# Kernel tuning notes

Hardware: AMD Instinct MI355X
Metric: run time of the kernel (lower is better)

Reference implementation:

```python
import jax, jax.numpy as jnp
import numpy as np
from jax import lax

B, T, HID = 4, 1024, 1024
H, DK, DV = 8, 128, 128
KCONV = 4
EPS = 1e-6
KEY_DIM = H * DK          # 1024
VAL_DIM = H * DV          # 1024
CONV_DIM = 2 * KEY_DIM + VAL_DIM  # 3072


def setup_inputs() -> dict:
    key = jax.random.key(0)
    ks = jax.random.split(key, 11)
    s = 0.02
    return {
        "hidden_states": jax.random.normal(ks[0], (B, T, HID), jnp.float32),
        "qkv_w": jax.random.normal(ks[1], (CONV_DIM, HID), jnp.float32) * s,
        "z_w": jax.random.normal(ks[2], (VAL_DIM, HID), jnp.float32) * s,
        "b_w": jax.random.normal(ks[3], (H, HID), jnp.float32) * s,
        "a_w": jax.random.normal(ks[4], (H, HID), jnp.float32) * s,
        "conv_w": jax.random.normal(ks[5], (CONV_DIM, 1, KCONV), jnp.float32) * 0.2,
        "dt_bias": jnp.ones((H,), jnp.float32),
        "A_log": jnp.log(jax.random.uniform(ks[6], (H,), jnp.float32, 1e-3, 16.0)),
        "norm_w": jnp.ones((DV,), jnp.float32),
        "out_w": jax.random.normal(ks[7], (HID, VAL_DIM), jnp.float32) * s,
    }


def reference(hidden_states, qkv_w, z_w, b_w, a_w, conv_w, dt_bias, A_log, norm_w, out_w):
    b_, t_, _ = hidden_states.shape

    # qkv projection -> [B, T, CONV_DIM]
    mixed = jnp.einsum("bth,ch->btc", hidden_states, qkv_w)

    # causal depthwise conv1d over time (groups == channels, padding K-1, truncated)
    x = mixed.transpose(0, 2, 1)  # [B, C, T]
    x = lax.conv_general_dilated(
        x, conv_w, window_strides=(1,), padding=[(KCONV - 1, 0)],
        feature_group_count=CONV_DIM,
        dimension_numbers=("NCH", "OIH", "NCH"))
    mixed = x.transpose(0, 2, 1)  # [B, T, C]

    z = jnp.einsum("bth,vh->btv", hidden_states, z_w).reshape(b_, t_, H, DV)
    bb = jnp.einsum("bth,nh->btn", hidden_states, b_w)   # [B,T,H]
    aa = jnp.einsum("bth,nh->btn", hidden_states, a_w)   # [B,T,H]

    q, k, v = jnp.split(mixed, 3, axis=-1)
    q = q.reshape(b_, t_, H, DK)
    k = k.reshape(b_, t_, H, DK)
    v = v.reshape(b_, t_, H, DV)

    beta = jax.nn.sigmoid(bb)                                  # [B,T,H]
    g = -jnp.exp(A_log) * jax.nn.softplus(aa + dt_bias)        # [B,T,H]
    alpha = jnp.exp(g)                                         # per-step decay

    # gated delta rule recurrence, time-major scan
    def step(S, inp):
        q_t, k_t, v_t, beta_t, alpha_t = inp  # [B,H,dk],[B,H,dk],[B,H,dv],[B,H],[B,H]
        S = S * alpha_t[..., None, None]                       # decay state
        kv = jnp.einsum("bhk,bhkv->bhv", k_t, S)              # retrieved memory
        S = S + jnp.einsum("bhk,bhv->bhkv", k_t, (v_t - kv) * beta_t[..., None])
        o_t = jnp.einsum("bhk,bhkv->bhv", q_t, S)
        return S, o_t

    qt = q.transpose(1, 0, 2, 3)
    kt = k.transpose(1, 0, 2, 3)
    vt = v.transpose(1, 0, 2, 3)
    bt = beta.transpose(1, 0, 2)
    at = alpha.transpose(1, 0, 2)
    S0 = jnp.zeros((b_, H, DK, DV), hidden_states.dtype)
    _, o = lax.scan(step, S0, (qt, kt, vt, bt, at))            # o: [T,B,H,dv]
    o = o.transpose(1, 0, 2, 3)                                # [B,T,H,dv]

    # gated RMSNorm: rmsnorm(o) * weight * silu(z)
    var = jnp.mean(jnp.square(o), axis=-1, keepdims=True)
    o = o * lax.rsqrt(var + EPS) * norm_w
    o = o * (z * jax.nn.sigmoid(z))

    out = jnp.einsum("btv,hv->bth", o.reshape(b_, t_, VAL_DIM), out_w)
    return out
```

## Files before the change

### kernel.cpp

```cpp
#include <hip/hip_runtime.h>

#define B_ 4
#define T_ 1024
#define HID_ 1024
#define H_ 8
#define CONV_DIM_ 3072
#define MROWS (B_*T_)

typedef __bf16 bf16x8 __attribute__((ext_vector_type(8)));
typedef float f32x4 __attribute__((ext_vector_type(4)));

#define MFMA16(a,b,c) __builtin_amdgcn_mfma_f32_16x16x32_bf16((a),(b),(c),0,0,0)

static __device__ __forceinline__ unsigned short f2bf(float f) {
  unsigned u = __float_as_uint(f);
  unsigned r = u + 0x7fffu + ((u >> 16) & 1u);
  return (unsigned short)(r >> 16);
}
static __device__ __forceinline__ float bfu2f(unsigned short v) {
  return __uint_as_float(((unsigned)v) << 16);
}
static __device__ __forceinline__ float4 recon4(ushort4 h, ushort4 l) {
  float4 r;
  r.x = bfu2f(h.x) + bfu2f(l.x);
  r.y = bfu2f(h.y) + bfu2f(l.y);
  r.z = bfu2f(h.z) + bfu2f(l.z);
  r.w = bfu2f(h.w) + bfu2f(l.w);
  return r;
}

static __device__ __forceinline__ void gld16(void* lds, const void* g) {
  __builtin_amdgcn_global_load_lds(
      (const __attribute__((address_space(1))) unsigned int*)g,
      (__attribute__((address_space(3))) unsigned int*)lds, 16, 0, 0);
}

__global__ __launch_bounds__(256) void f2bf_kernel(
    const float* __restrict__ src, unsigned short* __restrict__ dst, int n) {
  int i = (blockIdx.x * 256 + threadIdx.x) * 4;
  if (i >= n) return;
  float4 v = *(const float4*)(src + i);
  ushort4 o;
  o.x = f2bf(v.x); o.y = f2bf(v.y); o.z = f2bf(v.z); o.w = f2bf(v.w);
  *(ushort4*)(dst + i) = o;
}

__global__ __launch_bounds__(256) void f2bf_split_kernel(
    const float* __restrict__ src, unsigned short* __restrict__ hi,
    unsigned short* __restrict__ lo, int n) {
  int i = (blockIdx.x * 256 + threadIdx.x) * 4;
  if (i >= n) return;
  float4 v = *(const float4*)(src + i);
  ushort4 h, l;
  h.x = f2bf(v.x); h.y = f2bf(v.y); h.z = f2bf(v.z); h.w = f2bf(v.w);
  l.x = f2bf(v.x - bfu2f(h.x));
  l.y = f2bf(v.y - bfu2f(h.y));
  l.z = f2bf(v.z - bfu2f(h.z));
  l.w = f2bf(v.w - bfu2f(h.w));
  *(ushort4*)(hi + i) = h;
  *(ushort4*)(lo + i) = l;
}

template<int OUT_BF16>
__global__ __launch_bounds__(256) void gemm_mfma_kernel(
    const unsigned short* __restrict__ A, const unsigned short* __restrict__ W,
    void* __restrict__ Cv, int M, int N, int K) {
  __shared__ __align__(16) unsigned short lA[128*32];
  __shared__ __align__(16) unsigned short lB[128*32];
  const int tid  = threadIdx.x;
  const int lane = tid & 63;
  const int wv   = tid >> 6;
  const int wm   = (wv >> 1) * 64;
  const int wn   = (wv & 1) * 64;
  const int m16  = lane & 15;
  const int quad = lane >> 4;
  const int bm = blockIdx.y * 128;
  const int bn = blockIdx.x * 128;

  f32x4 acc[4][4];
  #pragma unroll
  for (int i = 0; i < 4; ++i)
    #pragma unroll
    for (int j = 0; j < 4; ++j)
      acc[i][j] = (f32x4){0.f, 0.f, 0.f, 0.f};

  const int r0 = tid >> 2, c0 = tid & 3;
  const int r1 = r0 + 64;
  const int g0 = (c0 ^ (r0 & 3)) * 8;
  const int g1 = (c0 ^ (r1 & 3)) * 8;
  const unsigned short* Ar0 = A + (size_t)(bm + r0) * K + g0;
  const unsigned short* Ar1 = A + (size_t)(bm + r1) * K + g1;
  const unsigned short* Wr0 = W + (size_t)(bn + r0) * K + g0;
  const unsigned short* Wr1 = W + (size_t)(bn + r1) * K + g1;
  unsigned short* sA0 = &lA[(size_t)tid * 8];
  unsigned short* sA1 = &lA[(size_t)(tid + 256) * 8];
  unsigned short* sB0 = &lB[(size_t)tid * 8];
  unsigned short* sB1 = &lB[(size_t)(tid + 256) * 8];

  int offA[4], offB[4];
  #pragma unroll
  for (int i = 0; i < 4; ++i) {
    int ra = wm + i * 16 + m16;
    offA[i] = ra * 32 + (quad ^ (ra & 3)) * 8;
    int rb = wn + i * 16 + m16;
    offB[i] = rb * 32 + (quad ^ (rb & 3)) * 8;
  }

  for (int k0 = 0; k0 < K; k0 += 32) {
    gld16(sA0, Ar0 + k0);
    gld16(sA1, Ar1 + k0);
    gld16(sB0, Wr0 + k0);
    gld16(sB1, Wr1 + k0);
    __syncthreads();
    bf16x8 af[4], bfr[4];
    #pragma unroll
    for (int i = 0; i < 4; ++i) {
      af[i]  = *(const bf16x8*)&lA[offA[i]];
      bfr[i] = *(const bf16x8*)&lB[offB[i]];
    }
    #pragma unroll
    for (int mi = 0; mi < 4; ++mi)
      #pragma unroll
      for (int ni = 0; ni < 4; ++ni)
        acc[mi][ni] = MFMA16(af[mi], bfr[ni], acc[mi][ni]);
    __syncthreads();
  }

  #pragma unroll
  for (int mi = 0; mi < 4; ++mi) {
    #pragma unroll
    for (int r = 0; r < 4; ++r) {
      size_t row = (size_t)(bm + wm + mi * 16 + quad * 4 + r);
      #pragma unroll
      for (int ni = 0; ni < 4; ++ni) {
        int col = bn + wn + ni * 16 + m16;
        float val = acc[mi][ni][r];
        if (OUT_BF16) ((unsigned short*)Cv)[row * N + col] = f2bf(val);
        else          ((float*)Cv)[row * N + col] = val;
      }
    }
  }
}

__global__ __launch_bounds__(256) void gemm_split_conv_kernel(
    const unsigned short* __restrict__ Ahi, const unsigned short* __restrict__ Alo,
    const unsigned short* __restrict__ Whi, const unsigned short* __restrict__ Wlo,
    const float* __restrict__ conv_w,
    unsigned short* __restrict__ qhi, unsigned short* __restrict__ qlo,
    unsigned short* __restrict__ khi, unsigned short* __restrict__ klo,
    float* __restrict__ vb, float* __restrict__ edge) {
  __shared__ __align__(16) unsigned char ldsraw[64*132*4 + 3*128*4];
  unsigned short* lAh = (unsigned short*)ldsraw;
  unsigned short* lAl = lAh + 128*32;
  unsigned short* lBh = lAl + 128*32;
  unsigned short* lBl = lBh + 128*32;
  float* smX2  = (float*)ldsraw;
  float* carry = (float*)(ldsraw + 64*132*4);

  const int tid  = threadIdx.x;
  const int lane = tid & 63;
  const int wv   = tid >> 6;
  const int wm   = (wv >> 1) * 64;
  const int wn   = (wv & 1) * 64;
  const int m16  = lane & 15;
  const int quad = lane >> 4;
  const int bm = blockIdx.y * 128;
  const int bn = blockIdx.x * 128;

  f32x4 acc[4][4];
  #pragma unroll
  for (int i = 0; i < 4; ++i)
    #pragma unroll
    for (int j = 0; j < 4; ++j)
      acc[i][j] = (f32x4){0.f, 0.f, 0.f, 0.f};

  const int r0 = tid >> 2, c0 = tid & 3;
  const int r1 = r0 + 64;
  const int g0 = (c0 ^ (r0 & 3)) * 8;
  const int g1 = (c0 ^ (r1 & 3)) * 8;
  const size_t oA0 = (size_t)(bm + r0) * 1024 + g0;
  const size_t oA1 = (size_t)(bm + r1) * 1024 + g1;
  const size_t oB0 = (size_t)(bn + r0) * 1024 + g0;
  const size_t oB1 = (size_t)(bn + r1) * 1024 + g1;
  const int s0 = tid * 8, s1 = (tid + 256) * 8;

  int offA[4], offB[4];
  #pragma unroll
  for (int i = 0; i < 4; ++i) {
    int ra = wm + i * 16 + m16;
    offA[i] = ra * 32 + (quad ^ (ra & 3)) * 8;
    int rb = wn + i * 16 + m16;
    offB[i] = rb * 32 + (quad ^ (rb & 3)) * 8;
  }

  for (int k0 = 0; k0 < 1024; k0 += 32) {
    gld16(&lAh[s0], Ahi + oA0 + k0);
    gld16(&lAh[s1], Ahi + oA1 + k0);
    gld16(&lAl[s0], Alo + oA0 + k0);
    gld16(&lAl[s1], Alo + oA1 + k0);
    gld16(&lBh[s0], Whi + oB0 + k0);
    gld16(&lBh[s1], Whi + oB1 + k0);
    gld16(&lBl[s0], Wlo + oB0 + k0);
    gld16(&lBl[s1], Wlo + oB1 + k0);
    __syncthreads();
    bf16x8 afh[4], bfh[4];
    #pragma unroll
    for (int i = 0; i < 4; ++i) {
      afh[i] = *(const bf16x8*)&lAh[offA[i]];
      bfh[i] = *(const bf16x8*)&lBh[offB[i]];
    }
    #pragma unroll
    for (int mi = 0; mi < 4; ++mi)
      #pragma unroll
      for (int ni = 0; ni < 4; ++ni)
        acc[mi][ni] = MFMA16(afh[mi], bfh[ni], acc[mi][ni]);
    {
      bf16x8 bfl[4];
      #pragma unroll
      for (int i = 0; i < 4; ++i) bfl[i] = *(const bf16x8*)&lBl[offB[i]];
      #pragma unroll
      for (int mi = 0; mi < 4; ++mi)
        #pragma unroll
        for (int ni = 0; ni < 4; ++ni)
          acc[mi][ni] = MFMA16(afh[mi], bfl[ni], acc[mi][ni]);
    }
    {
      bf16x8 afl[4];
      #pragma unroll
      for (int i = 0; i < 4; ++i) afl[i] = *(const bf16x8*)&lAl[offA[i]];
      #pragma unroll
      for (int mi = 0; mi < 4; ++mi)
        #pragma unroll
        for (int ni = 0; ni < 4; ++ni)
          acc[mi][ni] = MFMA16(afl[mi], bfh[ni], acc[mi][ni]);
    }
    __syncthreads();
  }

  const int bi = blockIdx.y;
  const int c  = tid & 127;
  const int rh = tid >> 7;
  const int cg = bn + c;
  const int part = cg >> 10;
  const int hh = (cg & 1023) >> 7;
  const int b = bm >> 10;
  const int tloc0 = bm & 1023;
  float4 w4 = *(const float4*)(conv_w + cg * 4);
  size_t rowb = ((size_t)(b * H_ + hh)) * T_;
  unsigned short* dh = (part == 0) ? qhi : khi;
  unsigned short* dl = (part == 0) ? qlo : klo;

  #pragma unroll
  for (int half = 0; half < 2; ++half) {
    if (half == 1) __syncthreads();
    if ((wv >> 1) == half) {
      #pragma unroll
      for (int mi = 0; mi < 4; ++mi)
        #pragma unroll
        for (int r = 0; r < 4; ++r) {
          int row = mi * 16 + quad * 4 + r;
          #pragma unroll
          for (int ni = 0; ni < 4; ++ni)
            smX2[row * 132 + wn + ni * 16 + m16] = acc[mi][ni][r];
        }
    }
    __syncthreads();
    if (half == 0) {
      #pragma unroll
      for (int e = 0; e < 2; ++e) {
        int idx = e * 256 + tid;
        int r = idx >> 7, cc = idx & 127;
        if (r < 3) {
          edge[((size_t)bi*6 + 3 + r)*3072 + bn + cc] = smX2[r*132 + cc];
          carry[r*128 + cc] = smX2[(61+r)*132 + cc];
        }
      }
    } else {
      if (bi < 31) {
        #pragma unroll
        for (int e = 0; e < 2; ++e) {
          int idx = e * 256 + tid;
          int r = idx >> 7, cc = idx & 127;
          if (r < 3)
            edge[((size_t)(bi+1)*6 + r)*3072 + bn + cc] = smX2[(61+r)*132 + cc];
        }
      }
    }
    {
      const int tb0 = rh * 32;
      float x0, x1, x2;
      if (tb0 >= 3) {
        x0 = smX2[(tb0-3)*132 + c];
        x1 = smX2[(tb0-2)*132 + c];
        x2 = smX2[(tb0-1)*132 + c];
      } else {
        if (half == 0) { x0 = 0.f; x1 = 0.f; x2 = 0.f; }
        else { x0 = carry[0*128 + c]; x1 = carry[1*128 + c]; x2 = carry[2*128 + c]; }
      }
      for (int tt = 0; tt < 32; ++tt) {
        const int t = tb0 + tt;
        float x3 = smX2[t*132 + c];
        float s = fmaf(w4.x, x0, fmaf(w4.y, x1, fmaf(w4.z, x2, w4.w * x3)));
        x0 = x1; x1 = x2; x2 = x3;
        const int tg = tloc0 + half*64 + t;
        if (part == 2) {
          vb[(rowb + tg) * 128 + c] = s;
        } else {
          int sw = (((c >> 3) ^ (tg & 7)) << 3) + (c & 7);
          unsigned short hv = f2bf(s);
          dh[(rowb + tg) * 128 + sw] = hv;
          dl[(rowb + tg) * 128 + sw] = f2bf(s - bfu2f(hv));
        }
      }
    }
  }
}

__global__ __launch_bounds__(128) void conv_fix_kernel(
    const float* __restrict__ edge, const float* __restrict__ conv_w,
    unsigned short* __restrict__ qhi, unsigned short* __restrict__ qlo,
    unsigned short* __restrict__ khi, unsigned short* __restrict__ klo,
    float* __restrict__ vb) {
  const int bi = blockIdx.x / 24;
  const int cb = blockIdx.x % 24;
  const int bm = bi * 128, n0 = cb * 128;
  const int b = bm >> 10, tloc = bm & 1023;
  const int c = threadIdx.x;
  const int cg = n0 + c;
  float m[6];
  #pragma unroll
  for (int j = 0; j < 6; ++j)
    m[j] = edge[((size_t)bi*6 + j)*3072 + cg];
  if (tloc == 0) { m[0] = 0.f; m[1] = 0.f; m[2] = 0.f; }
  const int part = cg >> 10;
  const int hh = (cg & 1023) >> 7;
  float4 w4 = *(const float4*)(conv_w + cg * 4);
  size_t rowb = ((size_t)(b * H_ + hh)) * T_;
  unsigned short* dh = (part == 0) ? qhi : khi;
  unsigned short* dl = (part == 0) ? qlo : klo;
  #pragma unroll
  for (int jo = 0; jo < 3; ++jo) {
    float s = fmaf(w4.x, m[jo], fmaf(w4.y, m[jo+1],
              fmaf(w4.z, m[jo+2], w4.w * m[jo+3])));
    const int tg = tloc + jo;
    if (part == 2) {
      vb[(rowb + tg) * 128 + c] = s;
    } else {
      int sw = (((c >> 3) ^ (tg & 7)) << 3) + (c & 7);
      unsigned short hv = f2bf(s);
      dh[(rowb + tg) * 128 + sw] = hv;
      dl[(rowb + tg) * 128 + sw] = f2bf(s - bfu2f(hv));
    }
  }
}

__global__ __launch_bounds__(128) void proj_ba_kernel(
    const float* __restrict__ hs, const float* __restrict__ b_w, const float* __restrict__ a_w,
    const float* __restrict__ dt_bias, const float* __restrict__ A_log,
    float* __restrict__ gout, float* __restrict__ beta,
    unsigned short* __restrict__ hs_hi, unsigned short* __restrict__ hs_lo) {
  const int bt = blockIdx.x;
  const int b = bt >> 10;
  const int t = bt & 1023;
  const int tid = threadIdx.x;
  const int grp = tid >> 3;
  const int l8 = tid & 7;
  const int h = grp & 7;
  const bool isA = grp >= 8;
  const float* w = (isA ? a_w : b_w) + (size_t)h * HID_;
  const float* x = hs + (size_t)bt * HID_;
  {
    const int e = tid * 8;
    float4 xv0 = *(const float4*)(x + e);
    float4 xv1 = *(const float4*)(x + e + 4);
    ushort4 h0, l0, h1, l1;
    h0.x = f2bf(xv0.x); h0.y = f2bf(xv0.y); h0.z = f2bf(xv0.z); h0.w = f2bf(xv0.w);
    l0.x = f2bf(xv0.x - bfu2f(h0.x)); l0.y = f2bf(xv0.y - bfu2f(h0.y));
    l0.z = f2bf(xv0.z - bfu2f(h0.z)); l0.w = f2bf(xv0.w - bfu2f(h0.w));
    h1.x = f2bf(xv1.x); h1.y = f2bf(xv1.y); h1.z = f2bf(xv1.z); h1.w = f2bf(xv1.w);
    l1.x = f2bf(xv1.x - bfu2f(h1.x)); l1.y = f2bf(xv1.y - bfu2f(h1.y));
    l1.z = f2bf(xv1.z - bfu2f(h1.z)); l1.w = f2bf(xv1.w - bfu2f(h1.w));
    unsigned short* hho = hs_hi + (size_t)bt * HID_ + e;
    unsigned short* hlo = hs_lo + (size_t)bt * HID_ + e;
    *(ushort4*)hho = h0;       *(ushort4*)hlo = l0;
    *(ushort4*)(hho + 4) = h1; *(ushort4*)(hlo + 4) = l1;
  }
  float s = 0.f;
  for (int e = l8*4; e < HID_; e += 32){
    float4 xv = *(const float4*)(x + e);
    float4 wv = *(const float4*)(w + e);
    s = fmaf(xv.x, wv.x, s);
    s = fmaf(xv.y, wv.y, s);
    s = fmaf(xv.z, wv.z, s);
    s = fmaf(xv.w, wv.w, s);
  }
  s += __shfl_xor(s,1); s += __shfl_xor(s,2); s += __shfl_xor(s,4);
  if (l8 == 0) {
    size_t o = ((size_t)(b*H_ + h))*T_ + t;
    if (!isA) {
      beta[o] = 1.f/(1.f+expf(-s));
    } else {
      float xx = s + dt_bias[h];
      float sp = fmaxf(xx,0.f) + log1pf(expf(-fabsf(xx)));
      gout[o] = -expf(A_log[h]) * sp;
    }
  }
}

__global__ __launch_bounds__(256) void scan_ab_kernel(
    const unsigned short* __restrict__ qhi_g, const unsigned short* __restrict__ qlo_g,
    const unsigned short* __restrict__ khi_g, const unsigned short* __restrict__ klo_g,
    const float* __restrict__ gbuf, const float* __restrict__ bbuf,
    unsigned short* __restrict__ Thi_g, unsigned short* __restrict__ Tlo_g,
    unsigned short* __restrict__ Bhi_g, unsigned short* __restrict__ Blo_g) {
  const int blk = blockIdx.x;
  const int bh = blk >> 4;
  const int ch = blk & 15;
  const int t0 = ch * 64;
  const int tid = threadIdx.x;
  __shared__ float sK[64][132];
  __shared__ float sAA[64][68];
  __shared__ float lL[64];
  __shared__ float bL[64];
  unsigned short* Tho = Thi_g + (size_t)blk*4096;
  unsigned short* Tlo = Tlo_g + (size_t)blk*4096;
  unsigned short* Bho = Bhi_g + (size_t)blk*4096;
  unsigned short* Blo = Blo_g + (size_t)blk*4096;

  #pragma unroll
  for (int i = 0; i < 8; ++i) {
    int f4 = tid + 256*i;
    int row = f4 >> 5, c4 = (f4 & 31) * 4;
    int gr = t0 + row;
    size_t base = ((size_t)bh*1024 + gr)*128;
    int sw = (((c4>>3) ^ (gr&7)) << 3) + (c4 & 7);
    ushort4 h = *(const ushort4*)&khi_g[base + sw];
    ushort4 l = *(const ushort4*)&klo_g[base + sw];
    *(float4*)&sK[row][c4] = recon4(h, l);
  }
  if (tid < 64) {
    float x = gbuf[(size_t)bh*T_ + t0 + tid];
    #pragma unroll
    for (int o = 1; o < 64; o <<= 1) {
      float y = __shfl_up(x, o);
      if (tid >= o) x += y;
    }
    lL[tid] = x;
    bL[tid] = bbuf[(size_t)bh*T_ + t0 + tid];
  }
  __syncthreads();

  const int it = tid >> 4, jt = tid & 15;
  {
    float acc[4][4] = {};
    if (jt <= it) {
      for (int kk = 0; kk < 128; kk += 4) {
        float4 ka[4], kc[4];
        #pragma unroll
        for (int r = 0; r < 4; ++r) {
          ka[r] = *(const float4*)&sK[it*4+r][kk];
          kc[r] = *(const float4*)&sK[jt*4+r][kk];
        }
        #pragma unroll
        for (int a = 0; a < 4; ++a)
          #pragma unroll
          for (int b = 0; b < 4; ++b) {
            acc[a][b] = fmaf(ka[a].x, kc[b].x, acc[a][b]);
            acc[a][b] = fmaf(ka[a].y, kc[b].y, acc[a][b]);
            acc[a][b] = fmaf(ka[a].z, kc[b].z, acc[a][b]);
            acc[a][b] = fmaf(ka[a].w, kc[b].w, acc[a][b]);
          }
      }
    }
    #pragma unroll
    for (int a = 0; a < 4; ++a) {
      int i = it*4 + a;
      float bi = bL[i], li = lL[i];
      #pragma unroll
      for (int b = 0; b < 4; ++b) {
        int j = jt*4 + b;
        sAA[i][j] = (j < i) ? bi * __expf(li - lL[j]) * acc[a][b] : 0.f;
      }
    }
  }
  {
    float acc[4][4] = {};
    if (jt <= it) {
      size_t qbase[4]; int qrx[4];
      #pragma unroll
      for (int r = 0; r < 4; ++r) {
        int gr = t0 + it*4 + r;
        qbase[r] = ((size_t)bh*1024 + gr)*128;
        qrx[r] = gr & 7;
      }
      for (int kk = 0; kk < 128; kk += 4) {
        float4 qa[4], kc[4];
        #pragma unroll
        for (int r = 0; r < 4; ++r) {
          int sw = (((kk>>3) ^ qrx[r]) << 3) + (kk & 7);
          ushort4 h = *(const ushort4*)&qhi_g[qbase[r] + sw];
          ushort4 l = *(const ushort4*)&qlo_g[qbase[r] + sw];
          qa[r] = recon4(h, l);
          kc[r] = *(const float4*)&sK[jt*4+r][kk];
        }
        #pragma unroll
        for (int a = 0; a < 4; ++a)
          #pragma unroll
          for (int b = 0; b < 4; ++b) {
            acc[a][b] = fmaf(qa[a].x, kc[b].x, acc[a][b]);
            acc[a][b] = fmaf(qa[a].y, kc[b].y, acc[a][b]);
            acc[a][b] = fmaf(qa[a].z, kc[b].z, acc[a][b]);
            acc[a][b] = fmaf(qa[a].w, kc[b].w, acc[a][b]);
          }
      }
    }
    #pragma unroll
    for (int a = 0; a < 4; ++a) {
      int i = it*4 + a;
      float li = lL[i];
      #pragma unroll
      for (int b = 0; b < 4; ++b) {
        int j = jt*4 + b;
        float x = (j <= i) ? __expf(li - lL[j]) * acc[a][b] : 0.f;
        unsigned short hv = f2bf(x);
        int sidx = i*64 + (((j>>3) ^ (i&7)) << 3) + (j&7);
        Bho[sidx] = hv;
        Blo[sidx] = f2bf(x - bfu2f(hv));
      }
    }
  }
  __syncthreads();

  {
    const int w = tid >> 6;
    const int ln = tid & 63;
    const int colc = w*16 + (ln & 15);
    const int rr = ln >> 4;
    float rh[16];
    #pragma unroll
    for (int m=0;m<16;++m) rh[m] = (rr + 4*m == colc) ? 1.f : 0.f;
    for (int j = 0; j < 63; ++j) {
      int src = ((j & 3) << 4) | (ln & 15);
      float wj = __shfl(rh[j >> 2], src);
      #pragma unroll
      for (int m=0;m<16;++m)
        rh[m] = fmaf(-sAA[rr + 4*m][j], wj, rh[m]);
    }
    #pragma unroll
    for (int m=0;m<16;++m) {
      int i2 = rr + 4*m;
      float x = rh[m];
      unsigned short hv = f2bf(x);
      int sidx = i2*64 + (((colc>>3) ^ (i2&7)) << 3) + (colc&7);
      Tho[sidx] = hv;
      Tlo[sidx] = f2bf(x - bfu2f(hv));
    }
  }
}

__global__ __launch_bounds__(512) void scan_seq_kernel(
    const unsigned short* __restrict__ khi_g, const unsigned short* __restrict__ klo_g,
    const unsigned short* __restrict__ qhi_g, const unsigned short* __restrict__ qlo_g,
    const float* __restrict__ vb,
    const float* __restrict__ gbuf, const float* __restrict__ bbuf,
    const unsigned short* __restrict__ Thi_g, const unsigned short* __restrict__ Tlo_g,
    const unsigned short* __restrict__ Bhi_g, const unsigned short* __restrict__ Blo_g,
    float* __restrict__ ob) {
  const int bh = blockIdx.x & 31;
  const int sl = blockIdx.x >> 5;
  const int tid = threadIdx.x;
  const int wv = tid >> 6;
  const int lane = tid & 63;
  const int v16 = lane & 15;
  const int quad = lane >> 4;
  const int tb = (wv & 3) * 16;
  const bool isQ = (wv >= 4);
  const int vx = v16 & 7;

  __shared__ __align__(16) unsigned short KhiL[2][64*128];
  __shared__ __align__(16) unsigned short KloL[2][64*128];
  __shared__ __align__(16) unsigned short WTh[16*64],  WTl[16*64];
  __shared__ __align__(16) unsigned short W2Th[16*64], W2Tl[16*64];
  __shared__ __align__(16) unsigned short W3Th[16*64], W3Tl[16*64];
  __shared__ __align__(16) unsigned short S0h[16*128], S0l[16*128];

  const unsigned short* kh  = khi_g + (size_t)bh*131072;
  const unsigned short* klp = klo_g + (size_t)bh*131072;
  const unsigned short* qh  = qhi_g + (size_t)bh*131072;
  const unsigned short* qlp = qlo_g + (size_t)bh*131072;
  const float* vg = vb + (size_t)bh*T_*128 + sl*16;
  const float* gg = gbuf + (size_t)bh*T_;
  const float* beg = bbuf + (size_t)bh*T_;
  float* og = ob + (size_t)bh*T_*128 + sl*16;

  f32x4 sreg = (f32x4){0.f, 0.f, 0.f, 0.f};
  const int kk0 = wv*16 + v16;
  const int k8 = kk0 >> 3, k7 = kk0 & 7;
  const int kq4 = (quad & 1) * 4;
  const int kr8 = (wv*16 + quad*4) >> 3;

  gld16(&KhiL[0][tid*8],        kh + tid*8);
  gld16(&KhiL[0][4096 + tid*8], kh + 4096 + tid*8);
  gld16(&KloL[0][tid*8],        klp + tid*8);
  gld16(&KloL[0][4096 + tid*8], klp + 4096 + tid*8);

  for (int ch = 0; ch < 16; ++ch) {
    const int t0 = ch * 64;
    const int cur = ch & 1;
    __syncthreads();

    if (ch < 15) {
      const size_t co = (size_t)(t0 + 64) * 128;
      gld16(&KhiL[cur^1][tid*8],        kh + co + tid*8);
      gld16(&KhiL[cur^1][4096 + tid*8], kh + co + 4096 + tid*8);
      gld16(&KloL[cur^1][tid*8],        klp + co + tid*8);
      gld16(&KloL[cur^1][4096 + tid*8], klp + co + 4096 + tid*8);
    }

    float gv = gg[t0 + lane];
    #pragma unroll
    for (int o = 1; o < 64; o <<= 1) {
      float y = __shfl_up(gv, o);
      if (lane >= o) gv += y;
    }
    float bv = beg[t0 + lane];

    const int ar = tb + v16;
    const int arx = ar & 7;
    const size_t tbo = ((size_t)(bh*16 + ch)) * 4096;
    bf16x8 tfh0, tfh1, tfl0, tfl1;
    bf16x8 bfh0, bfh1, bfl0, bfl1;
    bf16x8 qfh[4], qfl[4];
    if (!isQ) {
      int a0 = ar*64 + ((quad ^ arx) << 3);
      int a1 = ar*64 + (((4 + quad) ^ arx) << 3);
      tfh0 = *(const bf16x8*)&Thi_g[tbo + a0];
      tfh1 = *(const bf16x8*)&Thi_g[tbo + a1];
      tfl0 = *(const bf16x8*)&Tlo_g[tbo + a0];
      tfl1 = *(const bf16x8*)&Tlo_g[tbo + a1];
    } else {
      int a0 = ar*64 + ((quad ^ arx) << 3);
      int a1 = ar*64 + (((4 + quad) ^ arx) << 3);
      bfh0 = *(const bf16x8*)&Bhi_g[tbo + a0];
      bfh1 = *(const bf16x8*)&Bhi_g[tbo + a1];
      bfl0 = *(const bf16x8*)&Blo_g[tbo + a0];
      bfl1 = *(const bf16x8*)&Blo_g[tbo + a1];
      const size_t qco = (size_t)t0 * 128;
      #pragma unroll
      for (int ks = 0; ks < 4; ++ks) {
        int ao = ar*128 + (((4*ks + quad) ^ arx) << 3);
        qfh[ks] = *(const bf16x8*)&qh[qco + ao];
        qfl[ks] = *(const bf16x8*)&qlp[qco + ao];
      }
    }

    f32x4 facc = (f32x4){0.f,0.f,0.f,0.f};
    if (ch) {
      f32x4 f2 = (f32x4){0.f,0.f,0.f,0.f};
      #pragma unroll
      for (int ks = 0; ks < 4; ++ks) {
        const int u = 4*ks + quad;
        const int bo = v16*128 + ((u ^ vx) << 3);
        bf16x8 bhi = *(const bf16x8*)&S0h[bo];
        bf16x8 blo = *(const bf16x8*)&S0l[bo];
        bf16x8 ahi, alo;
        if (!isQ) {
          const int ao = ar*128 + ((u ^ arx) << 3);
          ahi = *(const bf16x8*)&KhiL[cur][ao];
          alo = *(const bf16x8*)&KloL[cur][ao];
        } else {
          ahi = qfh[ks]; alo = qfl[ks];
        }
        facc = MFMA16(ahi, bhi, facc);
        f2   = MFMA16(ahi, blo, f2);
        f2   = MFMA16(alo, bhi, f2);
      }
      facc[0] += f2[0]; facc[1] += f2[1]; facc[2] += f2[2]; facc[3] += f2[3];
    }
    const int t4 = tb + quad*4;
    const int wo = v16*64 + ((((t4>>3) ^ vx)) << 3) + (t4 & 7);
    f32x4 qacc = facc;
    if (!isQ) {
      float xr[4];
      #pragma unroll
      for (int r = 0; r < 4; ++r) {
        const int t = t4 + r;
        float be = __shfl(bv, t);
        float ga = __expf(__shfl(gv, t));
        float vvv = vg[(size_t)(t0 + t)*128 + v16];
        xr[r] = fmaf(-be*ga, facc[r], be*vvv);
      }
      ushort4 h4, l4;
      h4.x = f2bf(xr[0]); h4.y = f2bf(xr[1]); h4.z = f2bf(xr[2]); h4.w = f2bf(xr[3]);
      l4.x = f2bf(xr[0]-bfu2f(h4.x)); l4.y = f2bf(xr[1]-bfu2f(h4.y));
      l4.z = f2bf(xr[2]-bfu2f(h4.z)); l4.w = f2bf(xr[3]-bfu2f(h4.w));
      *(ushort4*)&WTh[wo] = h4;
      *(ushort4*)&WTl[wo] = l4;
    }
    __syncthreads();

    if (!isQ) {
      f32x4 wa = (f32x4){0.f,0.f,0.f,0.f};
      f32x4 wb = (f32x4){0.f,0.f,0.f,0.f};
      {
        const int b0 = v16*64 + ((quad ^ vx) << 3);
        const int b1 = v16*64 + (((4 + quad) ^ vx) << 3);
        bf16x8 r0h = *(const bf16x8*)&WTh[b0];
        bf16x8 r0l = *(const bf16x8*)&WTl[b0];
        bf16x8 r1h = *(const bf16x8*)&WTh[b1];
        bf16x8 r1l = *(const bf16x8*)&WTl[b1];
        wa = MFMA16(tfh0, r0h, wa);
        wb = MFMA16(tfh0, r0l, wb);
        wb = MFMA16(tfl0, r0h, wb);
        wa = MFMA16(tfh1, r1h, wa);
        wb = MFMA16(tfh1, r1l, wb);
        wb = MFMA16(tfl1, r1h, wb);
      }
      float Le = __shfl(gv, 63);
      float x0 = wa[0]+wb[0], x1 = wa[1]+wb[1], x2 = wa[2]+wb[2], x3 = wa[3]+wb[3];
      ushort4 h4, l4;
      h4.x = f2bf(x0); h4.y = f2bf(x1); h4.z = f2bf(x2); h4.w = f2bf(x3);
      l4.x = f2bf(x0-bfu2f(h4.x)); l4.y = f2bf(x1-bfu2f(h4.y));
      l4.z = f2bf(x2-bfu2f(h4.z)); l4.w = f2bf(x3-bfu2f(h4.w));
      *(ushort4*)&W2Th[wo] = h4;
      *(ushort4*)&W2Tl[wo] = l4;
      float w30 = x0 * __expf(Le - __shfl(gv, t4+0));
      float w31 = x1 * __expf(Le - __shfl(gv, t4+1));
      float w32 = x2 * __expf(Le - __shfl(gv, t4+2));
      float w33 = x3 * __expf(Le - __shfl(gv, t4+3));
      ushort4 h3, l3;
      h3.x = f2bf(w30); h3.y = f2bf(w31); h3.z = f2bf(w32); h3.w = f2bf(w33);
      l3.x = f2bf(w30-bfu2f(h3.x)); l3.y = f2bf(w31-bfu2f(h3.y));
      l3.z = f2bf(w32-bfu2f(h3.z)); l3.w = f2bf(w33-bfu2f(h3.w));
      *(ushort4*)&W3Th[wo] = h3;
      *(ushort4*)&W3Tl[wo] = l3;
    }
    __syncthreads();

    if (isQ) {
      f32x4 oa = (f32x4){0.f,0.f,0.f,0.f};
      f32x4 ob2 = (f32x4){0.f,0.f,0.f,0.f};
      const int b0 = v16*64 + ((quad ^ vx) << 3);
      const int b1 = v16*64 + (((4 + quad) ^ vx) << 3);
      bf16x8 w0h = *(const bf16x8*)&W2Th[b0];
      bf16x8 w0l = *(const bf16x8*)&W2Tl[b0];
      bf16x8 w1h = *(const bf16x8*)&W2Th[b1];
      bf16x8 w1l = *(const bf16x8*)&W2Tl[b1];
      oa  = MFMA16(bfh0, w0h, oa);
      ob2 = MFMA16(bfh0, w0l, ob2);
      ob2 = MFMA16(bfl0, w0h, ob2);
      oa  = MFMA16(bfh1, w1h, oa);
      ob2 = MFMA16(bfh1, w1l, ob2);
      ob2 = MFMA16(bfl1, w1h, ob2);
      #pragma unroll
      for (int r = 0; r < 4; ++r) {
        const int t = t4 + r;
        float ga = __expf(__shfl(gv, t));
        og[(size_t)(t0 + t)*128 + v16] = fmaf(ga, qacc[r], oa[r] + ob2[r]);
      }
    }

    if (ch != 15) {
      float gC = __expf(__shfl(gv, 63));
      sreg[0] *= gC; sreg[1] *= gC; sreg[2] *= gC; sreg[3] *= gC;
      f32x4 s2 = (f32x4){0.f,0.f,0.f,0.f};
      #pragma unroll
      for (int ks = 0; ks < 2; ++ks) {
        const int u = 4*ks + quad;
        const int tbase = u * 8;
        bf16x8 ahi, alo;
        #pragma unroll
        for (int j = 0; j < 8; ++j) {
          const int ad = (tbase + j)*128 + ((k8 ^ j) << 3) + k7;
          ahi[j] = *(const __bf16*)&KhiL[cur][ad];
          alo[j] = *(const __bf16*)&KloL[cur][ad];
        }
        const int bo = v16*64 + ((u ^ vx) << 3);
        bf16x8 bhi = *(const bf16x8*)&W3Th[bo];
        bf16x8 blo = *(const bf16x8*)&W3Tl[bo];
        sreg = MFMA16(ahi, bhi, sreg);
        s2   = MFMA16(ahi, blo, s2);
        s2   = MFMA16(alo, bhi, s2);
      }
      sreg[0] += s2[0]; sreg[1] += s2[1]; sreg[2] += s2[2]; sreg[3] += s2[3];
      const int so = v16*128 + ((kr8 ^ vx) << 3) + kq4;
      ushort4 h4, l4;
      h4.x = f2bf(sreg[0]); h4.y = f2bf(sreg[1]);
      h4.z = f2bf(sreg[2]); h4.w = f2bf(sreg[3]);
      l4.x = f2bf(sreg[0]-bfu2f(h4.x)); l4.y = f2bf(sreg[1]-bfu2f(h4.y));
      l4.z = f2bf(sreg[2]-bfu2f(h4.z)); l4.w = f2bf(sreg[3]-bfu2f(h4.w));
      *(ushort4*)&S0h[so] = h4;
      *(ushort4*)&S0l[so] = l4;
    }
  }
}

__global__ __launch_bounds__(256) void gnorm_kernel(
    const float* __restrict__ ob, const unsigned short* __restrict__ zbb,
    const float* __restrict__ norm_w, unsigned short* __restrict__ og) {
  const int tid = threadIdx.x;
  const int idx = blockIdx.x * 4 + (tid >> 6);
  const int lane = tid & 63;
  const int t = idx & 1023;
  const int bh = idx >> 10;
  const int b = bh >> 3;
  const int h = bh & 7;
  const float* o = ob + ((size_t)bh*T_ + t)*128;
  float2 ov = *(const float2*)(o + lane*2);
  float ss = fmaf(ov.x, ov.x, ov.y*ov.y);
  #pragma unroll
  for (int m=1; m<64; m<<=1) ss += __shfl_xor(ss, m);
  float inv = rsqrtf(ss*(1.f/128.f) + 1e-6f);
  size_t zoff = ((size_t)(b*T_+t))*1024 + (size_t)h*128 + lane*2;
  ushort2 zv = *(const ushort2*)(zbb + zoff);
  float z0 = bfu2f(zv.x), z1 = bfu2f(zv.y);
  float n0 = norm_w[lane*2], n1 = norm_w[lane*2+1];
  float r0 = ov.x*inv*n0 * z0/(1.f+expf(-z0));
  float r1 = ov.y*inv*n1 * z1/(1.f+expf(-z1));
  ushort2 ot;
  ot.x = f2bf(r0); ot.y = f2bf(r1);
  *(ushort2*)(og + zoff) = ot;
}

extern "C" void kernel_launch(void* const* d_in, const int* in_sizes, int n_in,
                              void* d_out, int out_size, void* d_ws, size_t ws_size,
                              hipStream_t stream) {
  const float* hs     = (const float*)d_in[0];
  const float* qkv_w  = (const float*)d_in[1];
  const float* z_w    = (const float*)d_in[2];
  const float* b_w    = (const float*)d_in[3];
  const float* a_w    = (const float*)d_in[4];
  const float* conv_w = (const float*)d_in[5];
  const float* dt_bias= (const float*)d_in[6];
  const float* A_log  = (const float*)d_in[7];
  const float* norm_w = (const float*)d_in[8];
  const float* out_w  = (const float*)d_in[9];
  float* out = (float*)d_out;

  char* wsp = (char*)d_ws;
  size_t off = 0;
  auto give = [&](size_t bytes)->char*{
    char* p = wsp + off; off += (bytes + 255) & ~(size_t)255; return p;
  };
  char* big    = give((size_t)MROWS*CONV_DIM_*4);
  unsigned short* zbuf = (unsigned short*)give((size_t)MROWS*1024*2);
  unsigned short* outw_bf = (unsigned short*)give((size_t)HID_*1024*2);
  char* bufA   = give((size_t)32*T_*128*4);
  char* bufB   = give((size_t)32*T_*128*4);
  char* bufC   = give((size_t)32*T_*128*4);
  float* gbuf  = (float*)give((size_t)32*T_*4);
  float* beta  = (float*)give((size_t)32*T_*4);

  unsigned short* khi = (unsigned short*)big;
  unsigned short* klo = khi + (size_t)4*1024*1024;
  unsigned short* qhi = klo + (size_t)4*1024*1024;
  unsigned short* qlo = qhi + (size_t)4*1024*1024;
  float* vdat = (float*)(qlo + (size_t)4*1024*1024);
  unsigned short* wz_bf = (unsigned short*)bufA;
  unsigned short* Blo_g = (unsigned short*)bufA + (size_t)1024*1024;
  unsigned short* og    = (unsigned short*)bufA + (size_t)3*1024*1024;
  float* edge           = (float*)(bufA + (size_t)10*1024*1024);
  unsigned short* hs_hi = (unsigned short*)bufB;
  unsigned short* hs_lo = hs_hi + (size_t)MROWS*HID_;
  unsigned short* Thi_g = (unsigned short*)bufB;
  unsigned short* Tlo_g = Thi_g + (size_t)512*4096;
  unsigned short* Bhi_g = Tlo_g + (size_t)512*4096;
  unsigned short* wc_hi = (unsigned short*)bufC;
  unsigned short* wc_lo = wc_hi + (size_t)CONV_DIM_*HID_;
  float* ob = (float*)bufC;

  f2bf_split_kernel<<<dim3(CONV_DIM_*HID_/1024), 256, 0, stream>>>(qkv_w, wc_hi, wc_lo, CONV_DIM_*HID_);
  f2bf_kernel<<<dim3(1024*HID_/1024), 256, 0, stream>>>(z_w, wz_bf, 1024*HID_);
  f2bf_kernel<<<dim3(1024*HID_/1024), 256, 0, stream>>>(out_w, outw_bf, 1024*HID_);
  proj_ba_kernel<<<dim3(MROWS), dim3(128), 0, stream>>>(
      hs, b_w, a_w, dt_bias, A_log, gbuf, beta, hs_hi, hs_lo);
  gemm_mfma_kernel<1><<<dim3(1024/128, MROWS/128), 256, 0, stream>>>(
      hs_hi, wz_bf, zbuf, MROWS, 1024, HID_);
  gemm_split_conv_kernel<<<dim3(CONV_DIM_/128, MROWS/128), 256, 0, stream>>>(
      hs_hi, hs_lo, wc_hi, wc_lo, conv_w, qhi, qlo, khi, klo, vdat, edge);
  conv_fix_kernel<<<dim3(32*24), dim3(128), 0, stream>>>(
      edge, conv_w, qhi, qlo, khi, klo, vdat);
  scan_ab_kernel<<<dim3(512), dim3(256), 0, stream>>>(
      qhi, qlo, khi, klo, gbuf, beta, Thi_g, Tlo_g, Bhi_g, Blo_g);
  scan_seq_kernel<<<dim3(256), dim3(512), 0, stream>>>(
      khi, klo, qhi, qlo, vdat, gbuf, beta, Thi_g, Tlo_g, Bhi_g, Blo_g, ob);
  gnorm_kernel<<<dim3(32*T_/4), dim3(256), 0, stream>>>(ob, zbuf, norm_w, og);
  gemm_mfma_kernel<0><<<dim3(1024/128, MROWS/128), 256, 0, stream>>>(og, outw_bf, out, MROWS, 1024, HID_);
}
```

Baseline: 363.0 us.

## Use split-bf16 MFMA for chunk KK^T/QK^T and merge weight conversions

```diff
diff --git a/kernel.cpp b/kernel.cpp
--- a/kernel.cpp
+++ b/kernel.cpp
@@ -35,30 +35,34 @@
       (__attribute__((address_space(3))) unsigned int*)lds, 16, 0, 0);
 }
 
-__global__ __launch_bounds__(256) void f2bf_kernel(
-    const float* __restrict__ src, unsigned short* __restrict__ dst, int n) {
-  int i = (blockIdx.x * 256 + threadIdx.x) * 4;
-  if (i >= n) return;
-  float4 v = *(const float4*)(src + i);
-  ushort4 o;
-  o.x = f2bf(v.x); o.y = f2bf(v.y); o.z = f2bf(v.z); o.w = f2bf(v.w);
-  *(ushort4*)(dst + i) = o;
-}
-
-__global__ __launch_bounds__(256) void f2bf_split_kernel(
-    const float* __restrict__ src, unsigned short* __restrict__ hi,
-    unsigned short* __restrict__ lo, int n) {
-  int i = (blockIdx.x * 256 + threadIdx.x) * 4;
-  if (i >= n) return;
-  float4 v = *(const float4*)(src + i);
-  ushort4 h, l;
-  h.x = f2bf(v.x); h.y = f2bf(v.y); h.z = f2bf(v.z); h.w = f2bf(v.w);
-  l.x = f2bf(v.x - bfu2f(h.x));
-  l.y = f2bf(v.y - bfu2f(h.y));
-  l.z = f2bf(v.z - bfu2f(h.z));
-  l.w = f2bf(v.w - bfu2f(h.w));
-  *(ushort4*)(hi + i) = h;
-  *(ushort4*)(lo + i) = l;
+__global__ __launch_bounds__(256) void convert_weights_kernel(
+    const float* __restrict__ qkv_w, const float* __restrict__ z_w,
+    const float* __restrict__ out_w,
+    unsigned short* __restrict__ wc_hi, unsigned short* __restrict__ wc_lo,
+    unsigned short* __restrict__ wz_bf, unsigned short* __restrict__ outw_bf) {
+  const int bid = blockIdx.x;
+  const int tid = threadIdx.x;
+  if (bid < 3072) {
+    int i = (bid * 256 + tid) * 4;
+    float4 v = *(const float4*)(qkv_w + i);
+    ushort4 h, l;
+    h.x = f2bf(v.x); h.y = f2bf(v.y); h.z = f2bf(v.z); h.w = f2bf(v.w);
+    l.x = f2bf(v.x - bfu2f(h.x));
+    l.y = f2bf(v.y - bfu2f(h.y));
+    l.z = f2bf(v.z - bfu2f(h.z));
+    l.w = f2bf(v.w - bfu2f(h.w));
+    *(ushort4*)(wc_hi + i) = h;
+    *(ushort4*)(wc_lo + i) = l;
+  } else {
+    const bool isZ = (bid < 4096);
+    const float* src = isZ ? z_w : out_w;
+    unsigned short* dst = isZ ? wz_bf : outw_bf;
+    int i = (((bid - (isZ ? 3072 : 4096)) * 256) + tid) * 4;
+    float4 v = *(const float4*)(src + i);
+    ushort4 o;
+    o.x = f2bf(v.x); o.y = f2bf(v.y); o.z = f2bf(v.z); o.w = f2bf(v.w);
+    *(ushort4*)(dst + i) = o;
+  }
 }
 
 template<int OUT_BF16>
@@ -418,7 +422,10 @@
   const int ch = blk & 15;
   const int t0 = ch * 64;
   const int tid = threadIdx.x;
-  __shared__ float sK[64][132];
+  const int wvb = tid >> 6;
+  const int lane = tid & 63;
+  const int v16 = lane & 15;
+  const int quad = lane >> 4;
   __shared__ float sAA[64][68];
   __shared__ float lL[64];
   __shared__ float bL[64];
@@ -426,18 +433,11 @@
   unsigned short* Tlo = Tlo_g + (size_t)blk*4096;
   unsigned short* Bho = Bhi_g + (size_t)blk*4096;
   unsigned short* Blo = Blo_g + (size_t)blk*4096;
-
-  #pragma unroll
-  for (int i = 0; i < 8; ++i) {
-    int f4 = tid + 256*i;
-    int row = f4 >> 5, c4 = (f4 & 31) * 4;
-    int gr = t0 + row;
-    size_t base = ((size_t)bh*1024 + gr)*128;
-    int sw = (((c4>>3) ^ (gr&7)) << 3) + (c4 & 7);
-    ushort4 h = *(const ushort4*)&khi_g[base + sw];
-    ushort4 l = *(const ushort4*)&klo_g[base + sw];
-    *(float4*)&sK[row][c4] = recon4(h, l);
-  }
+  const unsigned short* kh  = khi_g + (size_t)bh*131072 + (size_t)t0*128;
+  const unsigned short* klp = klo_g + (size_t)bh*131072 + (size_t)t0*128;
+  const unsigned short* qh  = qhi_g + (size_t)bh*131072 + (size_t)t0*128;
+  const unsigned short* qlp = qlo_g + (size_t)bh*131072 + (size_t)t0*128;
+
   if (tid < 64) {
     float x = gbuf[(size_t)bh*T_ + t0 + tid];
     #pragma unroll
@@ -448,84 +448,68 @@
     lL[tid] = x;
     bL[tid] = bbuf[(size_t)bh*T_ + t0 + tid];
   }
+
+  const int ar = wvb*16 + v16;
+  const int arx = ar & 7;
+  bf16x8 kAh[4], kAl[4], qAh[4], qAl[4];
+  #pragma unroll
+  for (int ks = 0; ks < 4; ++ks) {
+    const int u = 4*ks + quad;
+    const int ao = ar*128 + ((u ^ arx) << 3);
+    kAh[ks] = *(const bf16x8*)&kh[ao];
+    kAl[ks] = *(const bf16x8*)&klp[ao];
+    qAh[ks] = *(const bf16x8*)&qh[ao];
+    qAl[ks] = *(const bf16x8*)&qlp[ao];
+  }
   __syncthreads();
 
-  const int it = tid >> 4, jt = tid & 15;
-  {
-    float acc[4][4] = {};
-    if (jt <= it) {
-      for (int kk = 0; kk < 128; kk += 4) {
-        float4 ka[4], kc[4];
-        #pragma unroll
-        for (int r = 0; r < 4; ++r) {
-          ka[r] = *(const float4*)&sK[it*4+r][kk];
-          kc[r] = *(const float4*)&sK[jt*4+r][kk];
-        }
-        #pragma unroll
-        for (int a = 0; a < 4; ++a)
-          #pragma unroll
-          for (int b = 0; b < 4; ++b) {
-            acc[a][b] = fmaf(ka[a].x, kc[b].x, acc[a][b]);
-            acc[a][b] = fmaf(ka[a].y, kc[b].y, acc[a][b]);
-            acc[a][b] = fmaf(ka[a].z, kc[b].z, acc[a][b]);
-            acc[a][b] = fmaf(ka[a].w, kc[b].w, acc[a][b]);
-          }
-      }
-    }
-    #pragma unroll
-    for (int a = 0; a < 4; ++a) {
-      int i = it*4 + a;
-      float bi = bL[i], li = lL[i];
-      #pragma unroll
-      for (int b = 0; b < 4; ++b) {
-        int j = jt*4 + b;
-        sAA[i][j] = (j < i) ? bi * __expf(li - lL[j]) * acc[a][b] : 0.f;
-      }
-    }
-  }
-  {
-    float acc[4][4] = {};
-    if (jt <= it) {
-      size_t qbase[4]; int qrx[4];
+  const int i0 = wvb*16 + quad*4;
+  float biv[4], liv[4];
+  #pragma unroll
+  for (int r = 0; r < 4; ++r) { biv[r] = bL[i0+r]; liv[r] = lL[i0+r]; }
+
+  #pragma unroll
+  for (int cb = 0; cb < 4; ++cb) {
+    const int j = cb*16 + v16;
+    if (cb <= wvb) {
+      const int rb = cb*16 + v16;
+      const int rbx = rb & 7;
+      f32x4 a1 = (f32x4){0.f,0.f,0.f,0.f}, a2 = (f32x4){0.f,0.f,0.f,0.f};
+      f32x4 q1 = (f32x4){0.f,0.f,0.f,0.f}, q2 = (f32x4){0.f,0.f,0.f,0.f};
+      #pragma unroll
+      for (int ks = 0; ks < 4; ++ks) {
+        const int u = 4*ks + quad;
+        const int bo = rb*128 + ((u ^ rbx) << 3);
+        bf16x8 bhv = *(const bf16x8*)&kh[bo];
+        bf16x8 blv = *(const bf16x8*)&klp[bo];
+        a1 = MFMA16(kAh[ks], bhv, a1);
+        a2 = MFMA16(kAh[ks], blv, a2);
+        a2 = MFMA16(kAl[ks], bhv, a2);
+        q1 = MFMA16(qAh[ks], bhv, q1);
+        q2 = MFMA16(qAh[ks], blv, q2);
+        q2 = MFMA16(qAl[ks], bhv, q2);
+      }
+      float lj = lL[j];
       #pragma unroll
       for (int r = 0; r < 4; ++r) {
-        int gr = t0 + it*4 + r;
-        qbase[r] = ((size_t)bh*1024 + gr)*128;
-        qrx[r] = gr & 7;
-      }
-      for (int kk = 0; kk < 128; kk += 4) {
-        float4 qa[4], kc[4];
-        #pragma unroll
-        for (int r = 0; r < 4; ++r) {
-          int sw = (((kk>>3) ^ qrx[r]) << 3) + (kk & 7);
-          ushort4 h = *(const ushort4*)&qhi_g[qbase[r] + sw];
-          ushort4 l = *(const ushort4*)&qlo_g[qbase[r] + sw];
-          qa[r] = recon4(h, l);
-          kc[r] = *(const float4*)&sK[jt*4+r][kk];
-        }
-        #pragma unroll
-        for (int a = 0; a < 4; ++a)
-          #pragma unroll
-          for (int b = 0; b < 4; ++b) {
-            acc[a][b] = fmaf(qa[a].x, kc[b].x, acc[a][b]);
-            acc[a][b] = fmaf(qa[a].y, kc[b].y, acc[a][b]);
-            acc[a][b] = fmaf(qa[a].z, kc[b].z, acc[a][b]);
-            acc[a][b] = fmaf(qa[a].w, kc[b].w, acc[a][b]);
-          }
-      }
-    }
-    #pragma unroll
-    for (int a = 0; a < 4; ++a) {
-      int i = it*4 + a;
-      float li = lL[i];
-      #pragma unroll
-      for (int b = 0; b < 4; ++b) {
-        int j = jt*4 + b;
-        float x = (j <= i) ? __expf(li - lL[j]) * acc[a][b] : 0.f;
-        unsigned short hv = f2bf(x);
+        const int i = i0 + r;
+        float av = a1[r] + a2[r];
+        float qv = q1[r] + q2[r];
+        sAA[i][j] = (j < i) ? biv[r] * __expf(liv[r] - lj) * av : 0.f;
+        float xq = (j <= i) ? __expf(liv[r] - lj) * qv : 0.f;
+        unsigned short hv = f2bf(xq);
         int sidx = i*64 + (((j>>3) ^ (i&7)) << 3) + (j&7);
         Bho[sidx] = hv;
-        Blo[sidx] = f2bf(x - bfu2f(hv));
+        Blo[sidx] = f2bf(xq - bfu2f(hv));
+      }
+    } else {
+      #pragma unroll
+      for (int r = 0; r < 4; ++r) {
+        const int i = i0 + r;
+        sAA[i][j] = 0.f;
+        int sidx = i*64 + (((j>>3) ^ (i&7)) << 3) + (j&7);
+        Bho[sidx] = 0;
+        Blo[sidx] = 0;
       }
     }
   }
@@ -869,9 +853,8 @@
   unsigned short* wc_lo = wc_hi + (size_t)CONV_DIM_*HID_;
   float* ob = (float*)bufC;
 
-  f2bf_split_kernel<<<dim3(CONV_DIM_*HID_/1024), 256, 0, stream>>>(qkv_w, wc_hi, wc_lo, CONV_DIM_*HID_);
-  f2bf_kernel<<<dim3(1024*HID_/1024), 256, 0, stream>>>(z_w, wz_bf, 1024*HID_);
-  f2bf_kernel<<<dim3(1024*HID_/1024), 256, 0, stream>>>(out_w, outw_bf, 1024*HID_);
+  convert_weights_kernel<<<dim3(5120), 256, 0, stream>>>(
+      qkv_w, z_w, out_w, wc_hi, wc_lo, wz_bf, outw_bf);
   proj_ba_kernel<<<dim3(MROWS), dim3(128), 0, stream>>>(
       hs, b_w, a_w, dt_bias, A_log, gbuf, beta, hs_hi, hs_lo);
   gemm_mfma_kernel<1><<<dim3(1024/128, MROWS/128), 256, 0, stream>>>(
```

Result: faster. 339.2 us, median of 2 (-6.5%).
